# Performance work log

Measured on AMD Instinct MI355X. Metric: run time of the kernel, lower is better.

The kernel has to match this reference:

```python
import jax, jax.numpy as jnp
import numpy as np

L, H, D, DFF, B, S = 4, 8, 512, 2048, 2, 2048
DH = D // H
EPS = 1e-5
SCALE_BASE = 512.0


def setup_inputs() -> dict:
    key = jax.random.key(0)
    ks = jax.random.split(key, 8)
    def w(k, shape, s=0.02):
        return jax.random.normal(k, shape, jnp.float32) * s
    return {
        "x": jax.random.normal(ks[0], (B, S, D), jnp.float32),
        "WQ": w(ks[1], (L, H, D, DH)),
        "WK": w(ks[2], (L, H, D, DH)),
        "WV": w(ks[3], (L, H, D, DH)),
        "WG": w(ks[4], (L, D, D)),
        "WO": w(ks[5], (L, D, D)),
        "gn_w": jnp.ones((L, D), jnp.float32),
        "gn_b": jnp.zeros((L, D), jnp.float32),
        "ln1_w": jnp.ones((L, D), jnp.float32),
        "ln1_b": jnp.zeros((L, D), jnp.float32),
        "ln2_w": jnp.ones((L, D), jnp.float32),
        "ln2_b": jnp.zeros((L, D), jnp.float32),
        "ffn_w1": w(ks[6], (L, D, DFF)),
        "ffn_b1": jnp.zeros((L, DFF), jnp.float32),
        "ffn_w2": w(ks[7], (L, DFF, D)),
        "ffn_b2": jnp.zeros((L, D), jnp.float32),
    }


def _dup(t):
    # duplicate_interleave: [a,b] -> [a,a,b,b]
    return jnp.repeat(t, 2, axis=-1)


def _rot(x):
    # rotate_every_two: (x1,x2) -> (-x2, x1)
    x1, x2 = x[..., ::2], x[..., 1::2]
    return jnp.stack([-x2, x1], axis=-1).reshape(x.shape)


def _xpos(x, downscale):
    # x: [B,H,S,dh]  XPOS rotary with length-extrapolating scale
    s_len, dh = x.shape[-2], x.shape[-1]
    half = dh // 2
    base = (jnp.arange(0, dh, 2, dtype=jnp.float32) + 0.4 * dh) / (1.4 * dh)  # [half]
    power = jnp.arange(s_len, dtype=jnp.float32) / SCALE_BASE
    scale = base[None, :] ** power[:, None]  # [S, half]
    if downscale:
        scale = 1.0 / scale
    inv_freq = 1.0 / (10000.0 ** (jnp.arange(half, dtype=jnp.float32) / half))
    ang = jnp.arange(s_len, dtype=jnp.float32)[:, None] * inv_freq[None, :]
    sin, cos, sc = _dup(jnp.sin(ang)), _dup(jnp.cos(ang)), _dup(scale)
    return x * cos * sc + _rot(x) * sin * sc


def _ln(x, w, b):
    mu = jnp.mean(x, -1, keepdims=True)
    var = jnp.mean((x - mu) ** 2, -1, keepdims=True)
    return (x - mu) * jax.lax.rsqrt(var + EPS) * w + b


def reference(x, WQ, WK, WV, WG, WO, gn_w, gn_b, ln1_w, ln1_b, ln2_w, ln2_b, ffn_w1, ffn_b1, ffn_w2, ffn_b2):
    gammas = 1.0 - jnp.exp(jnp.linspace(np.log(1.0 / 32.0), np.log(1.0 / 512.0), H)).astype(jnp.float32)
    idx = jnp.arange(S, dtype=jnp.float32)
    diff = idx[:, None] - idx[None, :]
    Dmask = jnp.where(diff >= 0, gammas[:, None, None] ** diff, 0.0)  # [H,S,S]
    b = x.shape[0]
    for i in range(L):
        xn = _ln(x, ln1_w[i], ln1_b[i])
        q = _xpos(jnp.einsum('bsd,hde->bhse', xn, WQ[i]), False)
        k = _xpos(jnp.einsum('bsd,hde->bhse', xn, WK[i]), True)
        v = jnp.einsum('bsd,hde->bhse', xn, WV[i])
        att = jnp.einsum('bhse,bhte->bhst', q, k) * Dmask[None]  # [B,H,S,S]
        yh = jnp.einsum('bhst,bhte->bhse', att, v)               # [B,H,S,dh]
        yh = yh.transpose(0, 2, 1, 3)                            # [B,S,H,dh]
        mu = jnp.mean(yh, -1, keepdims=True)
        var = jnp.mean((yh - mu) ** 2, -1, keepdims=True)
        yn = (yh - mu) * jax.lax.rsqrt(var + EPS)
        yn = yn * gn_w[i].reshape(H, DH) + gn_b[i].reshape(H, DH)
        y = yn.reshape(b, S, D)
        g = jax.nn.silu(xn @ WG[i])
        y1 = (g * y) @ WO[i] + x
        h = _ln(y1, ln2_w[i], ln2_b[i])
        x = jax.nn.gelu(h @ ffn_w1[i] + ffn_b1[i], approximate=False) @ ffn_w2[i] + ffn_b2[i] + y1
    return x
```

## Files before the change

### kernel.cpp

```cpp
#include <hip/hip_runtime.h>
#include <hip/hip_bf16.h>

#define LYR 4
#define NH  8
#define DM  512
#define DHD 64
#define DFF 2048
#define BB  2
#define SSL 2048
#define NROWS (BB*SSL)

typedef unsigned short u16;
typedef __attribute__((ext_vector_type(8))) short bf16x8;
typedef __attribute__((ext_vector_type(4))) float f32x4;
typedef __attribute__((ext_vector_type(4))) unsigned int u32x4;

__device__ __forceinline__ u16 f2bf(float f) {
    union { float f; unsigned u; } v; v.f = f;
    unsigned r = v.u + 0x7FFFu + ((v.u >> 16) & 1u);
    return (u16)(r >> 16);
}
__device__ __forceinline__ float bf2f(u16 b) {
    union { unsigned u; float f; } v; v.u = ((unsigned)b) << 16;
    return v.f;
}
__device__ __forceinline__ int swz(int row, int col) {
    return row * 64 + (col & 7) + ((((col >> 3) ^ row) & 7) << 3);
}
__device__ __forceinline__ int swzP(int row, int col) {
    return row * 128 + (col & 7) + ((((col >> 3) ^ row) & 15) << 3);
}
__device__ __forceinline__ void gload16(const u16* g, u16* l) {
    __builtin_amdgcn_global_load_lds(
        (const __attribute__((address_space(1))) unsigned int*)g,
        (__attribute__((address_space(3))) unsigned int*)l, 16, 0, 0);
}


__global__ __launch_bounds__(256) void xpos_tables(float* __restrict__ tab) {
    const int idx = blockIdx.x * 256 + threadIdx.x;
    const int s = idx >> 5, j = idx & 31;
    const float base = (2.f * j + 0.4f * 64.f) / (1.4f * 64.f);
    const float invf = powf(10000.f, -(float)j / 32.f);
    const float ang = (float)s * invf;
    const float scq = powf(base, (float)s / 512.f);
    tab[idx]          = sinf(ang);
    tab[idx + 65536]  = cosf(ang);
    tab[idx + 131072] = scq;
    tab[idx + 196608] = 1.f / scq;
}

__global__ __launch_bounds__(256)
void prep_qkv(const float* __restrict__ WQp, const float* __restrict__ WKp,
              const float* __restrict__ WVp, u16* __restrict__ WBT) {
    const int dt = blockIdx.x;
    const int h = blockIdx.y & 7, which = blockIdx.y >> 3;
    const int l = blockIdx.z;
    const float* W = (which == 0 ? WQp : which == 1 ? WKp : WVp);
    const float* ip = W + ((size_t)(l * 8 + h)) * (512 * 64);
    u16* op = WBT + (size_t)l * (2048 * 512) + (size_t)(which * 512 + h * 64) * 512;
    __shared__ u16 tile[64 * 72];
    const int t = threadIdx.x, rr = t >> 2, cc = (t & 3) * 16;
    const float* src = ip + (size_t)(dt * 64 + rr) * 64 + cc;
#pragma unroll
    for (int i = 0; i < 16; ++i) tile[rr * 72 + cc + i] = f2bf(src[i]);
    __syncthreads();
    u16 tmp[16] __attribute__((aligned(16)));
#pragma unroll
    for (int i = 0; i < 16; ++i) tmp[i] = tile[(cc + i) * 72 + rr];
    u16* dst = op + (size_t)rr * 512 + dt * 64 + cc;
    *(u32x4*)&dst[0] = *(const u32x4*)&tmp[0];
    *(u32x4*)&dst[8] = *(const u32x4*)&tmp[8];
}

__global__ __launch_bounds__(256)
void prep_t(const float* __restrict__ in, u16* __restrict__ out, int R, int C,
            long long in_ls, long long out_ls) {
    const float* ip = in + (size_t)blockIdx.z * in_ls;
    u16* op = out + (size_t)blockIdx.z * out_ls;
    const int r0 = blockIdx.x * 64, c0t = blockIdx.y * 64;
    __shared__ u16 tile[64 * 72];
    const int t = threadIdx.x, rr = t >> 2, cc = (t & 3) * 16;
    const float* src = ip + (size_t)(r0 + rr) * C + c0t + cc;
#pragma unroll
    for (int i = 0; i < 16; ++i) tile[rr * 72 + cc + i] = f2bf(src[i]);
    __syncthreads();
    u16 tmp[16] __attribute__((aligned(16)));
#pragma unroll
    for (int i = 0; i < 16; ++i) tmp[i] = tile[(cc + i) * 72 + rr];
    u16* dst = op + (size_t)(c0t + rr) * R + r0 + cc;
    *(u32x4*)&dst[0] = *(const u32x4*)&tmp[0];
    *(u32x4*)&dst[8] = *(const u32x4*)&tmp[8];
}

__global__ __launch_bounds__(256)
void ln_kernel(const float* __restrict__ x, const float* __restrict__ wt,
               const float* __restrict__ bs, u16* __restrict__ out) {
    const int row = blockIdx.x * 4 + (threadIdx.x >> 6);
    const int lane = threadIdx.x & 63;
    const float* xr = x + (size_t)row * DM + lane * 8;
    float v[8];
    *(float4*)&v[0] = *(const float4*)&xr[0];
    *(float4*)&v[4] = *(const float4*)&xr[4];
    float s = 0.f, s2 = 0.f;
#pragma unroll
    for (int i = 0; i < 8; ++i) { s += v[i]; s2 += v[i] * v[i]; }
#pragma unroll
    for (int m = 1; m < 64; m <<= 1) {
        s  += __shfl_xor(s, m, 64);
        s2 += __shfl_xor(s2, m, 64);
    }
    const float mu = s * (1.f / DM);
    const float rs = rsqrtf(s2 * (1.f / DM) - mu * mu + 1e-5f);
    const int e0 = lane * 8;
    u16 o[8] __attribute__((aligned(16)));
#pragma unroll
    for (int i = 0; i < 8; ++i)
        o[i] = f2bf((v[i] - mu) * rs * wt[e0 + i] + bs[e0 + i]);
    *(u32x4*)&out[(size_t)row * DM + e0] = *(const u32x4*)o;
}

template <int BM, int BN, int EPI>
__global__ __launch_bounds__(256)
void gemm_bt(const u16* __restrict__ A, const u16* __restrict__ Bt,
             u16* __restrict__ obf, float* __restrict__ of32,
             const float* __restrict__ res, const float* __restrict__ bias,
             int M, int N, int K) {
    constexpr int FM = BM / 32, FN = BN / 32;
    __shared__ __align__(16) u16 As[BM * 64];
    __shared__ __align__(16) u16 Bs[BN * 64];
    const int t = threadIdx.x;
    const int lane = t & 63, w4 = t >> 6;
    const int wr = w4 >> 1, wc = w4 & 1;
    const int fr = lane & 15, fq = lane >> 4;
    const int m0 = blockIdx.y * BM, n0 = blockIdx.x * BN;
    const int lr = lane >> 3;
    const int ls = lane & 7;
    f32x4 acc[FM][FN] = {};
    for (int k0 = 0; k0 < K; k0 += 64) {
#pragma unroll
        for (int q = 0; q < BM / 32; ++q) {
            const int ib = q * 4 + w4;
            const int row = ib * 8 + lr;
            const int cc = ls ^ (row & 7);
            gload16(&A[(size_t)(m0 + row) * K + k0 + cc * 8], &As[ib * 512]);
        }
#pragma unroll
        for (int q = 0; q < BN / 32; ++q) {
            const int ib = q * 4 + w4;
            const int row = ib * 8 + lr;
            const int cc = ls ^ (row & 7);
            gload16(&Bt[(size_t)(n0 + row) * K + k0 + cc * 8], &Bs[ib * 512]);
        }
        __syncthreads();
#pragma unroll
        for (int ks = 0; ks < 2; ++ks) {
            bf16x8 av[FM], bv[FN];
#pragma unroll
            for (int i = 0; i < FM; ++i)
                av[i] = *(const bf16x8*)&As[swz(wr * (BM / 2) + i * 16 + fr, ks * 32 + fq * 8)];
#pragma unroll
            for (int j = 0; j < FN; ++j)
                bv[j] = *(const bf16x8*)&Bs[swz(wc * (BN / 2) + j * 16 + fr, ks * 32 + fq * 8)];
#pragma unroll
            for (int i = 0; i < FM; ++i)
#pragma unroll
                for (int j = 0; j < FN; ++j)
                    acc[i][j] = __builtin_amdgcn_mfma_f32_16x16x32_bf16(av[i], bv[j], acc[i][j], 0, 0, 0);
        }
        __syncthreads();
    }
#pragma unroll
    for (int i = 0; i < FM; ++i)
#pragma unroll
        for (int j = 0; j < FN; ++j)
#pragma unroll
            for (int r = 0; r < 4; ++r) {
                const int m = m0 + wr * (BM / 2) + i * 16 + fq * 4 + r;
                const int n = n0 + wc * (BN / 2) + j * 16 + fr;
                const size_t idx = (size_t)m * N + n;
                float v = acc[i][j][r];
                if constexpr (EPI == 0) {
                    obf[idx] = f2bf(v);
                } else if constexpr (EPI == 1) {
                    of32[idx] = v + res[idx];
                } else if constexpr (EPI == 2) {
                    float tt = v + bias[n];
                    obf[idx] = f2bf(0.5f * tt * (1.f + erff(tt * 0.7071067811865475f)));
                } else {
                    of32[idx] = v + bias[n] + res[idx];
                }
            }
}

__global__ __launch_bounds__(256)
void xpos_relayout(const u16* __restrict__ qkvg, const float* __restrict__ tab,
                   u16* __restrict__ Qb, u16* __restrict__ Kb, u16* __restrict__ Vt) {
    const int st = blockIdx.x, h = blockIdx.y, b = blockIdx.z;
    const int t = threadIdx.x;
    const int r = t >> 2;
    const int sg = st * 64 + r;
    const size_t rawrow = ((size_t)(b * SSL + sg)) * 2048;
    const size_t qrow = ((size_t)((b * NH + h) * SSL + sg)) * 64;
    const int j0 = (t & 3) * 8;
#pragma unroll
    for (int jj = 0; jj < 8; ++jj) {
        const int j = j0 + jj;
        const float sn = tab[sg * 32 + j];
        const float cs = tab[sg * 32 + j + 65536];
        const float sq = tab[sg * 32 + j + 131072];
        const float sk2 = tab[sg * 32 + j + 196608];
        unsigned rawq = *(const unsigned*)&qkvg[rawrow + h * 64 + 2 * j];
        float q0 = bf2f((u16)(rawq & 0xffff)), q1 = bf2f((u16)(rawq >> 16));
        float o0 = (q0 * cs - q1 * sn) * sq;
        float o1 = (q1 * cs + q0 * sn) * sq;
        *(unsigned*)&Qb[qrow + 2 * j] = ((unsigned)f2bf(o1) << 16) | (unsigned)f2bf(o0);
        unsigned rawk = *(const unsigned*)&qkvg[rawrow + 512 + h * 64 + 2 * j];
        float k0 = bf2f((u16)(rawk & 0xffff)), k1 = bf2f((u16)(rawk >> 16));
        float p0 = (k0 * cs - k1 * sn) * sk2;
        float p1 = (k1 * cs + k0 * sn) * sk2;
        *(unsigned*)&Kb[qrow + 2 * j] = ((unsigned)f2bf(p1) << 16) | (unsigned)f2bf(p0);
    }
    __shared__ __align__(16) u16 vt[64 * 72];
    const int c0 = (t & 3) * 16;
    *(u32x4*)&vt[r * 72 + c0]     = *(const u32x4*)&qkvg[rawrow + 1024 + h * 64 + c0];
    *(u32x4*)&vt[r * 72 + c0 + 8] = *(const u32x4*)&qkvg[rawrow + 1024 + h * 64 + c0 + 8];
    __syncthreads();
    u16 tmp[16] __attribute__((aligned(16)));
#pragma unroll
    for (int i = 0; i < 16; ++i) tmp[i] = vt[(c0 + i) * 72 + r];
    u16* dst = Vt + ((size_t)((b * NH + h) * 64 + r)) * SSL + st * 64 + c0;
    *(u32x4*)&dst[0] = *(const u32x4*)&tmp[0];
    *(u32x4*)&dst[8] = *(const u32x4*)&tmp[8];
}

__global__ __launch_bounds__(512)
void retention(const u16* __restrict__ Qb, const u16* __restrict__ Kb,
               const u16* __restrict__ Vt, const u16* __restrict__ qkvg,
               const float* __restrict__ gnw, const float* __restrict__ gnb,
               u16* __restrict__ zb) {
    extern __shared__ __align__(16) char smem[];
    u16* KsB = (u16*)smem;
    u16* VsB = (u16*)(smem + 32768);
    u16* Qs  = (u16*)(smem + 65536);
    u16* Ps  = (u16*)(smem + 73728);

    const int bid = blockIdx.x;
    const int qt = 31 - (bid >> 4);
    const int bh = bid & 15;
    const int h = bh & 7, b = bh >> 3;
    const int t = threadIdx.x;
    const int lane = t & 63, w = t >> 6;
    const int fr = lane & 15, fq = lane >> 4;
    const int wr = w & 1, wc2 = w >> 1;
    const int oc = wc2 & 1, th = w >> 2;

    const float gamma = 1.f - expf(-3.4657359f + (float)h * -0.39608410f);
    const float lgam = log2f(gamma);
    const float dlim = 19.931568f / (-lgam);
    const int jt_last = (qt * 64 + 63) >> 7;
    int jt_min = 0;
    {
        const float need = (float)(qt * 64 - 127) - dlim;
        if (need > 0.f) jt_min = (int)ceilf(need * (1.f / 128.f));
        if (jt_min > jt_last) jt_min = jt_last;
        if (jt_min < 0) jt_min = 0;
    }

    float rowf[2][4], colf[2];
#pragma unroll
    for (int i = 0; i < 2; ++i)
#pragma unroll
        for (int rr = 0; rr < 4; ++rr)
            rowf[i][rr] = exp2f((float)(wr * 32 + i * 16 + fq * 4 + rr) * lgam);
#pragma unroll
    for (int j = 0; j < 2; ++j)
        colf[j] = exp2f(-(float)(wc2 * 32 + j * 16 + fr) * lgam);

    const size_t bh2048 = (size_t)bh * 2048;
    const int lr8 = lane >> 3, ls8 = lane & 7;
    const int lr16 = lane >> 4, ls16 = lane & 15;

    {
        const int row = w * 8 + lr8;
        const int cc = ls8 ^ (row & 7);
        gload16(&Qb[(bh2048 + qt * 64 + row) * 64 + cc * 8], &Qs[w * 512]);
    }

    f32x4 oacc[2][2] = {};
    int cur = 0;
    {
        const int jt = jt_min;
        u16* Kd = KsB; u16* Vd = VsB;
#pragma unroll
        for (int q = 0; q < 2; ++q) {
            const int row = q * 64 + w * 8 + lr8;
            const int cc = ls8 ^ (row & 7);
            gload16(&Kb[(bh2048 + jt * 128 + row) * 64 + cc * 8], &Kd[(q * 64 + w * 8) * 64]);
        }
#pragma unroll
        for (int q = 0; q < 2; ++q) {
            const int row = w * 8 + q * 4 + lr16;
            const int cc = ls16 ^ (row & 15);
            gload16(&Vt[((size_t)bh * 64 + row) * 2048 + jt * 128 + cc * 8], &Vd[(w * 8 + q * 4) * 128]);
        }
    }

    for (int jt = jt_min; jt <= jt_last; ++jt) {
        __syncthreads();
        if (jt < jt_last) {
            const int nb = cur ^ 1;
            u16* Kd = KsB + nb * 8192;
            u16* Vd = VsB + nb * 8192;
#pragma unroll
            for (int q = 0; q < 2; ++q) {
                const int row = q * 64 + w * 8 + lr8;
                const int cc = ls8 ^ (row & 7);
                gload16(&Kb[(bh2048 + (jt + 1) * 128 + row) * 64 + cc * 8], &Kd[(q * 64 + w * 8) * 64]);
            }
#pragma unroll
            for (int q = 0; q < 2; ++q) {
                const int row = w * 8 + q * 4 + lr16;
                const int cc = ls16 ^ (row & 15);
                gload16(&Vt[((size_t)bh * 64 + row) * 2048 + (jt + 1) * 128 + cc * 8], &Vd[(w * 8 + q * 4) * 128]);
            }
        }
        const u16* Kc = KsB + cur * 8192;
        f32x4 sac[2][2] = {};
#pragma unroll
        for (int ks = 0; ks < 2; ++ks) {
            bf16x8 qa[2], kb[2];
#pragma unroll
            for (int i = 0; i < 2; ++i)
                qa[i] = *(const bf16x8*)&Qs[swz(wr * 32 + i * 16 + fr, ks * 32 + fq * 8)];
#pragma unroll
            for (int j = 0; j < 2; ++j)
                kb[j] = *(const bf16x8*)&Kc[swz(wc2 * 32 + j * 16 + fr, ks * 32 + fq * 8)];
#pragma unroll
            for (int i = 0; i < 2; ++i)
#pragma unroll
                for (int j = 0; j < 2; ++j)
                    sac[i][j] = __builtin_amdgcn_mfma_f32_16x16x32_bf16(qa[i], kb[j], sac[i][j], 0, 0, 0);
        }
        const float sc = exp2f((float)(qt * 64 - jt * 128) * lgam);
        const bool diag = (jt == jt_last);
#pragma unroll
        for (int i = 0; i < 2; ++i)
#pragma unroll
            for (int j = 0; j < 2; ++j)
#pragma unroll
                for (int rr = 0; rr < 4; ++rr) {
                    float m = sc * rowf[i][rr] * colf[j];
                    if (diag) {
                        const int d = (qt * 64 + wr * 32 + i * 16 + fq * 4 + rr)
                                    - (jt * 128 + wc2 * 32 + j * 16 + fr);
                        if (d < 0) m = 0.f;
                    }
                    Ps[swzP(wr * 32 + i * 16 + fq * 4 + rr, wc2 * 32 + j * 16 + fr)] =
                        f2bf(sac[i][j][rr] * m);
                }
        __syncthreads();
        const u16* Vc = VsB + cur * 8192;
#pragma unroll
        for (int ks = 0; ks < 2; ++ks) {
            const int tcol = th * 64 + ks * 32 + fq * 8;
            bf16x8 pa[2], vb[2];
#pragma unroll
            for (int i = 0; i < 2; ++i)
                pa[i] = *(const bf16x8*)&Ps[swzP(wr * 32 + i * 16 + fr, tcol)];
#pragma unroll
            for (int j = 0; j < 2; ++j)
                vb[j] = *(const bf16x8*)&Vc[swzP(oc * 32 + j * 16 + fr, tcol)];
#pragma unroll
            for (int i = 0; i < 2; ++i)
#pragma unroll
                for (int j = 0; j < 2; ++j)
                    oacc[i][j] = __builtin_amdgcn_mfma_f32_16x16x32_bf16(pa[i], vb[j], oacc[i][j], 0, 0, 0);
        }
        cur ^= 1;
    }

    __syncthreads();
    float* Of = (float*)smem;
    if (th == 1) {
#pragma unroll
        for (int i = 0; i < 2; ++i)
#pragma unroll
            for (int j = 0; j < 2; ++j)
#pragma unroll
                for (int rr = 0; rr < 4; ++rr)
                    Of[(wr * 32 + i * 16 + fq * 4 + rr) * 66 + oc * 32 + j * 16 + fr] = oacc[i][j][rr];
    }
    __syncthreads();
    if (th == 0) {
#pragma unroll
        for (int i = 0; i < 2; ++i)
#pragma unroll
            for (int j = 0; j < 2; ++j)
#pragma unroll
                for (int rr = 0; rr < 4; ++rr) {
                    const int idx = (wr * 32 + i * 16 + fq * 4 + rr) * 66 + oc * 32 + j * 16 + fr;
                    Of[idx] += oacc[i][j][rr];
                }
    }
    __syncthreads();
    const int row = t >> 3, c0 = (t & 7) * 8;
    float v[8];
    float s = 0.f, s2 = 0.f;
#pragma unroll
    for (int i = 0; i < 8; ++i) {
        v[i] = Of[row * 66 + c0 + i];
        s += v[i]; s2 += v[i] * v[i];
    }
    s  += __shfl_xor(s, 1, 64);  s  += __shfl_xor(s, 2, 64);  s  += __shfl_xor(s, 4, 64);
    s2 += __shfl_xor(s2, 1, 64); s2 += __shfl_xor(s2, 2, 64); s2 += __shfl_xor(s2, 4, 64);
    const float mu = s * (1.f / 64.f);
    const float rs = rsqrtf(s2 * (1.f / 64.f) - mu * mu + 1e-5f);
    const int sg = qt * 64 + row;
    u16 gv[8] __attribute__((aligned(16)));
    *(u32x4*)gv = *(const u32x4*)&qkvg[((size_t)(b * SSL + sg)) * 2048 + 1536 + h * 64 + c0];
    u16 ob[8] __attribute__((aligned(16)));
#pragma unroll
    for (int i = 0; i < 8; ++i) {
        const int dc = h * 64 + c0 + i;
        const float yn = (v[i] - mu) * rs * gnw[dc] + gnb[dc];
        const float g = bf2f(gv[i]);
        ob[i] = f2bf(yn * (g / (1.f + expf(-g))));
    }
    *(u32x4*)&zb[((size_t)(b * SSL + sg)) * 512 + h * 64 + c0] = *(const u32x4*)ob;
}

extern "C" void kernel_launch(void* const* d_in, const int* in_sizes, int n_in,
                              void* d_out, int out_size, void* d_ws, size_t ws_size,
                              hipStream_t stream) {
    const float* X    = (const float*)d_in[0];
    const float* WQ   = (const float*)d_in[1];
    const float* WK   = (const float*)d_in[2];
    const float* WV   = (const float*)d_in[3];
    const float* WG   = (const float*)d_in[4];
    const float* WO   = (const float*)d_in[5];
    const float* GNW  = (const float*)d_in[6];
    const float* GNB  = (const float*)d_in[7];
    const float* LN1W = (const float*)d_in[8];
    const float* LN1B = (const float*)d_in[9];
    const float* LN2W = (const float*)d_in[10];
    const float* LN2B = (const float*)d_in[11];
    const float* FW1  = (const float*)d_in[12];
    const float* FB1  = (const float*)d_in[13];
    const float* FW2  = (const float*)d_in[14];
    const float* FB2  = (const float*)d_in[15];

    char* ws = (char*)d_ws;
    size_t off = 0;
    auto alloc = [&](size_t n) { char* p = ws + off; off += (n + 255) & ~(size_t)255; return p; };

    u16*   WBT  = (u16*)alloc((size_t)LYR * 2048 * 512 * 2);
    u16*   WOT  = (u16*)alloc((size_t)LYR * 512 * 512 * 2);
    u16*   W1T  = (u16*)alloc((size_t)LYR * 2048 * 512 * 2);
    u16*   W2T  = (u16*)alloc((size_t)LYR * 512 * 2048 * 2);
    float* TAB  = (float*)alloc((size_t)4 * 2048 * 32 * 4);
    float* XB   = (float*)alloc((size_t)NROWS * DM * 4);
    u16*   XN   = (u16*)alloc((size_t)NROWS * DM * 2);
    u16*   QKVG = (u16*)alloc((size_t)NROWS * 2048 * 2);
    u16*   QBp  = (u16*)alloc((size_t)NROWS * DM * 2);
    u16*   KBp  = (u16*)alloc((size_t)NROWS * DM * 2);
    u16*   VTp  = (u16*)alloc((size_t)NROWS * DM * 2);
    u16*   ZB   = (u16*)alloc((size_t)NROWS * DM * 2);
    float* Y1   = (float*)alloc((size_t)NROWS * DM * 4);
    u16*   HB   = QBp;
    u16*   FF1  = QKVG;

    xpos_tables<<<256, 256, 0, stream>>>(TAB);
    prep_qkv<<<dim3(8, 24, LYR), 256, 0, stream>>>(WQ, WK, WV, WBT);
    prep_t<<<dim3(8, 8, LYR), 256, 0, stream>>>(WG, WBT + 1536 * 512, 512, 512,
                                                (long long)512 * 512, (long long)2048 * 512);
    prep_t<<<dim3(8, 8, LYR), 256, 0, stream>>>(WO, WOT, 512, 512,
                                                (long long)512 * 512, (long long)512 * 512);
    prep_t<<<dim3(8, 32, LYR), 256, 0, stream>>>(FW1, W1T, 512, 2048,
                                                 (long long)512 * 2048, (long long)2048 * 512);
    prep_t<<<dim3(32, 8, LYR), 256, 0, stream>>>(FW2, W2T, 2048, 512,
                                                 (long long)2048 * 512, (long long)512 * 2048);

    for (int l = 0; l < LYR; ++l) {
        const float* xsrc = (l == 0) ? X : XB;
        float* xdst = (l == LYR - 1) ? (float*)d_out : XB;
        ln_kernel<<<NROWS / 4, 256, 0, stream>>>(xsrc, LN1W + l * 512, LN1B + l * 512, XN);
        gemm_bt<128, 128, 0><<<dim3(16, 32), 256, 0, stream>>>(
            XN, WBT + (size_t)l * 2048 * 512, QKVG, nullptr, nullptr, nullptr, NROWS, 2048, 512);
        xpos_relayout<<<dim3(SSL / 64, NH, BB), 256, 0, stream>>>(QKVG, TAB, QBp, KBp, VTp);
        retention<<<512, 512, 90112, stream>>>(QBp, KBp, VTp, QKVG,
                                               GNW + l * 512, GNB + l * 512, ZB);
        gemm_bt<64, 128, 1><<<dim3(4, 64), 256, 0, stream>>>(
            ZB, WOT + (size_t)l * 512 * 512, nullptr, Y1, xsrc, nullptr, NROWS, 512, 512);
        ln_kernel<<<NROWS / 4, 256, 0, stream>>>(Y1, LN2W + l * 512, LN2B + l * 512, HB);
        gemm_bt<128, 128, 2><<<dim3(16, 32), 256, 0, stream>>>(
            HB, W1T + (size_t)l * 2048 * 512, FF1, nullptr, nullptr, FB1 + l * 2048, NROWS, 2048, 512);
        gemm_bt<64, 128, 3><<<dim3(4, 64), 256, 0, stream>>>(
            FF1, W2T + (size_t)l * 512 * 2048, nullptr, xdst, Y1, FB2 + l * 512, NROWS, 512, 2048);
    }
}
```

Baseline: 526.7 us.

## Double-buffer GEMM LDS tiles and remap workgroups across XCDs

The GEMM kernel now keeps two LDS stages and prefetches tile k+2 with global_load_lds while MFMAs consume tile k, replacing the load-then-sync loop with explicit vmcnt waits and barriers. Workgroup IDs in the GEMMs and the retention kernel are remapped so consecutive blocks on the same XCD (blockIdx mod 8) work on neighbouring tiles, which is meant to improve L2 locality. Grids become 1-D to match. This doubles GEMM LDS use, which may lower occupancy, and the hand-written waitcnt counts must match the number of issued loads exactly.

```diff
diff --git a/kernel.cpp b/kernel.cpp
--- a/kernel.cpp
+++ b/kernel.cpp
@@ -34,6 +34,16 @@
     __builtin_amdgcn_global_load_lds(
         (const __attribute__((address_space(1))) unsigned int*)g,
         (__attribute__((address_space(3))) unsigned int*)l, 16, 0, 0);
+}
+template <int N> __device__ __forceinline__ void wait_vmcnt() {
+    if constexpr (N == 0)      asm volatile("s_waitcnt vmcnt(0)" ::: "memory");
+    else if constexpr (N == 6) asm volatile("s_waitcnt vmcnt(6)" ::: "memory");
+    else if constexpr (N == 8) asm volatile("s_waitcnt vmcnt(8)" ::: "memory");
+    else static_assert(N == 0 || N == 6 || N == 8, "unsupported vmcnt");
+}
+__device__ __forceinline__ void block_barrier() {
+    __builtin_amdgcn_s_barrier();
+    asm volatile("" ::: "memory");
 }
 
 
@@ -127,48 +137,67 @@
              const float* __restrict__ res, const float* __restrict__ bias,
              int M, int N, int K) {
     constexpr int FM = BM / 32, FN = BN / 32;
-    __shared__ __align__(16) u16 As[BM * 64];
-    __shared__ __align__(16) u16 Bs[BN * 64];
+    constexpr int LPS = BM / 32 + BN / 32;
+    __shared__ __align__(16) u16 As[2][BM * 64];
+    __shared__ __align__(16) u16 Bs[2][BN * 64];
     const int t = threadIdx.x;
     const int lane = t & 63, w4 = t >> 6;
     const int wr = w4 >> 1, wc = w4 & 1;
     const int fr = lane & 15, fq = lane >> 4;
-    const int m0 = blockIdx.y * BM, n0 = blockIdx.x * BN;
+    const int nX = N / BN;
+    const int nwg = (M / BM) * nX;
+    const int swzid = (blockIdx.x & 7) * (nwg >> 3) + (blockIdx.x >> 3);
+    const int m0 = (swzid / nX) * BM, n0 = (swzid % nX) * BN;
     const int lr = lane >> 3;
     const int ls = lane & 7;
-    f32x4 acc[FM][FN] = {};
-    for (int k0 = 0; k0 < K; k0 += 64) {
+    const int nsteps = K >> 6;
+
+    auto stage = [&](int step, int slot) {
+        const int k0 = step << 6;
 #pragma unroll
         for (int q = 0; q < BM / 32; ++q) {
             const int ib = q * 4 + w4;
             const int row = ib * 8 + lr;
             const int cc = ls ^ (row & 7);
-            gload16(&A[(size_t)(m0 + row) * K + k0 + cc * 8], &As[ib * 512]);
+            gload16(&A[(size_t)(m0 + row) * K + k0 + cc * 8], &As[slot][ib * 512]);
         }
 #pragma unroll
         for (int q = 0; q < BN / 32; ++q) {
             const int ib = q * 4 + w4;
             const int row = ib * 8 + lr;
             const int cc = ls ^ (row & 7);
-            gload16(&Bt[(size_t)(n0 + row) * K + k0 + cc * 8], &Bs[ib * 512]);
-        }
-        __syncthreads();
+            gload16(&Bt[(size_t)(n0 + row) * K + k0 + cc * 8], &Bs[slot][ib * 512]);
+        }
+    };
+
+    f32x4 acc[FM][FN] = {};
+    stage(0, 0);
+    stage(1, 1);
+    for (int st = 0; st < nsteps; ++st) {
+        if (st + 1 < nsteps) wait_vmcnt<LPS>(); else wait_vmcnt<0>();
+        __builtin_amdgcn_sched_barrier(0);
+        block_barrier();
+        const u16* Ac = As[st & 1];
+        const u16* Bc = Bs[st & 1];
 #pragma unroll
         for (int ks = 0; ks < 2; ++ks) {
             bf16x8 av[FM], bv[FN];
 #pragma unroll
             for (int i = 0; i < FM; ++i)
-                av[i] = *(const bf16x8*)&As[swz(wr * (BM / 2) + i * 16 + fr, ks * 32 + fq * 8)];
+                av[i] = *(const bf16x8*)&Ac[swz(wr * (BM / 2) + i * 16 + fr, ks * 32 + fq * 8)];
 #pragma unroll
             for (int j = 0; j < FN; ++j)
-                bv[j] = *(const bf16x8*)&Bs[swz(wc * (BN / 2) + j * 16 + fr, ks * 32 + fq * 8)];
+                bv[j] = *(const bf16x8*)&Bc[swz(wc * (BN / 2) + j * 16 + fr, ks * 32 + fq * 8)];
 #pragma unroll
             for (int i = 0; i < FM; ++i)
 #pragma unroll
                 for (int j = 0; j < FN; ++j)
                     acc[i][j] = __builtin_amdgcn_mfma_f32_16x16x32_bf16(av[i], bv[j], acc[i][j], 0, 0, 0);
         }
-        __syncthreads();
+        asm volatile("s_waitcnt lgkmcnt(0)" ::: "memory");
+        __builtin_amdgcn_sched_barrier(0);
+        block_barrier();
+        if (st + 2 < nsteps) stage(st + 2, st & 1);
     }
 #pragma unroll
     for (int i = 0; i < FM; ++i)
@@ -245,9 +274,9 @@
     u16* Qs  = (u16*)(smem + 65536);
     u16* Ps  = (u16*)(smem + 73728);
 
-    const int bid = blockIdx.x;
-    const int qt = 31 - (bid >> 4);
-    const int bh = bid & 15;
+    const int logical = (blockIdx.x & 7) * 64 + (blockIdx.x >> 3);
+    const int bh = logical >> 5;
+    const int qt = 31 - (logical & 31);
     const int h = bh & 7, b = bh >> 3;
     const int t = threadIdx.x;
     const int lane = t & 63, w = t >> 6;
@@ -485,17 +514,17 @@
         const float* xsrc = (l == 0) ? X : XB;
         float* xdst = (l == LYR - 1) ? (float*)d_out : XB;
         ln_kernel<<<NROWS / 4, 256, 0, stream>>>(xsrc, LN1W + l * 512, LN1B + l * 512, XN);
-        gemm_bt<128, 128, 0><<<dim3(16, 32), 256, 0, stream>>>(
+        gemm_bt<128, 128, 0><<<512, 256, 0, stream>>>(
             XN, WBT + (size_t)l * 2048 * 512, QKVG, nullptr, nullptr, nullptr, NROWS, 2048, 512);
         xpos_relayout<<<dim3(SSL / 64, NH, BB), 256, 0, stream>>>(QKVG, TAB, QBp, KBp, VTp);
         retention<<<512, 512, 90112, stream>>>(QBp, KBp, VTp, QKVG,
                                                GNW + l * 512, GNB + l * 512, ZB);
-        gemm_bt<64, 128, 1><<<dim3(4, 64), 256, 0, stream>>>(
+        gemm_bt<64, 128, 1><<<256, 256, 0, stream>>>(
             ZB, WOT + (size_t)l * 512 * 512, nullptr, Y1, xsrc, nullptr, NROWS, 512, 512);
         ln_kernel<<<NROWS / 4, 256, 0, stream>>>(Y1, LN2W + l * 512, LN2B + l * 512, HB);
-        gemm_bt<128, 128, 2><<<dim3(16, 32), 256, 0, stream>>>(
+        gemm_bt<128, 128, 2><<<512, 256, 0, stream>>>(
             HB, W1T + (size_t)l * 2048 * 512, FF1, nullptr, nullptr, FB1 + l * 2048, NROWS, 2048, 512);
-        gemm_bt<64, 128, 3><<<dim3(4, 64), 256, 0, stream>>>(
+        gemm_bt<64, 128, 3><<<256, 256, 0, stream>>>(
             FF1, W2T + (size_t)l * 512 * 2048, nullptr, xdst, Y1, FB2 + l * 512, NROWS, 512, 2048);
     }
 }
```

Measured after the change: 475.0 us. -9.8%, faster.
